# Performance work log

Measured on AMD Instinct MI355X. Metric: run time of the kernel, lower is better.

The kernel has to match this reference:

```python
import jax, jax.numpy as jnp
import numpy as np

DIM = 1024
HEADS = 16
HEAD_DIM = DIM // HEADS


def setup_inputs() -> dict:
    key = jax.random.key(0)
    k_x, k_qkv, k_ow, k_ob = jax.random.split(key, 4)
    x = jax.random.normal(k_x, (2, 2048, DIM), dtype=jnp.float32)
    # nn.Linear(dim, 3*dim, bias=False): weight shape [3*dim, dim], y = x @ W.T
    w_qkv = jax.random.normal(k_qkv, (3 * DIM, DIM), dtype=jnp.float32) * (DIM ** -0.5)
    # nn.Linear(dim, dim) with bias
    w_o = jax.random.normal(k_ow, (DIM, DIM), dtype=jnp.float32) * (DIM ** -0.5)
    b_o = jax.random.normal(k_ob, (DIM,), dtype=jnp.float32) * 0.02
    return {"x": x, "w_qkv": w_qkv, "w_o": w_o, "b_o": b_o}


def reference(x, w_qkv, w_o, b_o):
    b, n, _ = x.shape
    scale = DIM ** -0.5  # NOTE: source scales by full dim, not head dim
    # qkv projection: [b, n, 3*dim]
    qkv = jnp.einsum('bnd,ed->bne', x, w_qkv)
    # 'b n (qkv h d) -> qkv b h n d'
    qkv = qkv.reshape(b, n, 3, HEADS, HEAD_DIM)
    q = jnp.transpose(qkv[:, :, 0], (0, 2, 1, 3))  # [b, h, n, d]
    k = jnp.transpose(qkv[:, :, 1], (0, 2, 1, 3))
    v = jnp.transpose(qkv[:, :, 2], (0, 2, 1, 3))
    scores = jnp.einsum('bhqd,bhkd->bhqk', q, k) * scale  # [b, h, n, n]
    attn = jax.nn.softmax(scores, axis=-1)
    out = jnp.einsum('bhqk,bhkd->bhqd', attn, v)  # [b, h, n, d]
    out = jnp.transpose(out, (0, 2, 1, 3)).reshape(b, n, DIM)  # 'b h n d -> b n (h d)'
    out = jnp.einsum('bnd,ed->bne', out, w_o) + b_o
    return out
```

## Files before the change

kernel.cpp:

```cpp
#include <hip/hip_runtime.h>
#include <stdint.h>


#define DIM 1024
#define SEQ 2048
#define BATCH 2
#define ROWS 4096
#define RSTRIDE 3072

typedef __bf16 bf16_t;
typedef bf16_t bf16x4 __attribute__((ext_vector_type(4)));
typedef bf16_t bf16x8 __attribute__((ext_vector_type(8)));
typedef float f32x4 __attribute__((ext_vector_type(4)));

__device__ __forceinline__ ushort f2bf(float f) {
    uint32_t u;
    __builtin_memcpy(&u, &f, 4);
    uint32_t r = (u + 0x7fffu + ((u >> 16) & 1u)) >> 16;
    return (ushort)r;
}

__device__ __forceinline__ void store_out(ushort* p, float v) { *p = f2bf(v); }
__device__ __forceinline__ void store_out(float* p, float v) { *p = v; }

__device__ __forceinline__ void gl_lds16(const void* g, void* l) {
    __builtin_amdgcn_global_load_lds(
        (const __attribute__((address_space(1))) void*)g,
        (__attribute__((address_space(3))) void*)l, 16, 0, 0);
}

__global__ __launch_bounds__(256) void cvt_kernel(
    const float* __restrict__ src, ushort* __restrict__ dst) {
    int i = (blockIdx.x * 256 + threadIdx.x) * 8;
    float4 a = *(const float4*)(src + i);
    float4 b = *(const float4*)(src + i + 4);
    uint4 u;
    u.x = (uint)f2bf(a.x) | ((uint)f2bf(a.y) << 16);
    u.y = (uint)f2bf(a.z) | ((uint)f2bf(a.w) << 16);
    u.z = (uint)f2bf(b.x) | ((uint)f2bf(b.y) << 16);
    u.w = (uint)f2bf(b.z) | ((uint)f2bf(b.w) << 16);
    *(uint4*)(dst + i) = u;
}

template <typename OutT>
__global__ __launch_bounds__(256) void gemm_bt_kernel(
    const ushort* __restrict__ A, const ushort* __restrict__ B,
    const float* __restrict__ bias, OutT* __restrict__ C,
    int M, int N, int K) {
    __shared__ __align__(16) ushort sA[128 * 32];
    __shared__ __align__(16) ushort sB[128 * 32];

    const int tid = threadIdx.x;
    const int lane = tid & 63, w = tid >> 6;
    const int quad = lane >> 4, l15 = lane & 15;
    const int wm = (w >> 1) * 64, wn = (w & 1) * 64;
    const int bm = blockIdx.y, bn = blockIdx.x;

    f32x4 acc[4][4];
#pragma unroll
    for (int i = 0; i < 4; i++)
#pragma unroll
        for (int j = 0; j < 4; j++) acc[i][j] = (f32x4){0.f, 0.f, 0.f, 0.f};

    const ushort* Abase = A + (size_t)(bm * 128) * K;
    const ushort* Bbase = B + (size_t)(bn * 128) * K;
    const int rr = lane >> 2, c16 = lane & 3;

    for (int kk = 0; kk < K; kk += 32) {
        __syncthreads();
#pragma unroll
        for (int t = 0; t < 2; t++) {
            int row = w * 32 + t * 16;
            gl_lds16(Abase + (size_t)(row + rr) * K + kk + c16 * 8, sA + row * 32);
            gl_lds16(Bbase + (size_t)(row + rr) * K + kk + c16 * 8, sB + row * 32);
        }
        __syncthreads();

        bf16x8 af[4], bfr[4];
#pragma unroll
        for (int i = 0; i < 4; i++)
            af[i] = *(const bf16x8*)((const bf16_t*)sA + (wm + i * 16 + l15) * 32 + quad * 8);
#pragma unroll
        for (int j = 0; j < 4; j++)
            bfr[j] = *(const bf16x8*)((const bf16_t*)sB + (wn + j * 16 + l15) * 32 + quad * 8);
#pragma unroll
        for (int i = 0; i < 4; i++)
#pragma unroll
            for (int j = 0; j < 4; j++)
                acc[i][j] = __builtin_amdgcn_mfma_f32_16x16x32_bf16(
                    af[i], bfr[j], acc[i][j], 0, 0, 0);
    }

#pragma unroll
    for (int i = 0; i < 4; i++)
#pragma unroll
        for (int j = 0; j < 4; j++) {
            int col = bn * 128 + wn + j * 16 + l15;
            float bv = bias ? bias[col] : 0.f;
#pragma unroll
            for (int r = 0; r < 4; r++) {
                int row = bm * 128 + wm + i * 16 + quad * 4 + r;
                store_out(&C[(size_t)row * N + col], acc[i][j][r] + bv);
            }
        }
}

__global__ __launch_bounds__(512) void flash_attn_kernel(
    const ushort* __restrict__ qkv, ushort* __restrict__ out) {
    __shared__ __align__(16) ushort sK[64 * 72];
    __shared__ __align__(16) ushort sVt[64 * 72];
    __shared__ __align__(16) ushort sP[128 * 68];

    const int tid = threadIdx.x;
    const int lane = tid & 63, w = tid >> 6;
    const int quad = lane >> 4, l15 = lane & 15;
    const int bh = blockIdx.y, b = bh >> 4, h = bh & 15;
    const int q0 = blockIdx.x * 128;
    const ushort* qkvb = qkv + (size_t)b * SEQ * RSTRIDE + h * 64;

    const ushort* qrow = qkvb + (size_t)(q0 + w * 16 + l15) * RSTRIDE;
    const bf16x8 aq0 = *(const bf16x8*)(qrow + quad * 8);
    const bf16x8 aq1 = *(const bf16x8*)(qrow + 32 + quad * 8);

    const int krow = tid >> 3, kc8 = tid & 7;
    const int vrp = tid & 31, vc4 = tid >> 5;

    uint4 kreg;
    ushort4 va, vb;
    {
        kreg = *(const uint4*)(qkvb + (size_t)krow * RSTRIDE + DIM + kc8 * 8);
        const ushort* v0 = qkvb + (size_t)(2 * vrp) * RSTRIDE + 2 * DIM + vc4 * 4;
        va = *(const ushort4*)v0;
        vb = *(const ushort4*)(v0 + RSTRIDE);
    }

    f32x4 l_acc = (f32x4){0.f, 0.f, 0.f, 0.f};
    f32x4 o[4];
#pragma unroll
    for (int j = 0; j < 4; j++) o[j] = (f32x4){0.f, 0.f, 0.f, 0.f};

    bf16x8 vones;
#pragma unroll
    for (int e = 0; e < 8; e++) vones[e] = (bf16_t)1.0f;

    const float c_exp = 0.04508422f;

    uint* vt32 = (uint*)sVt;
    for (int kb = 0; kb < SEQ; kb += 64) {
        *(uint4*)(sK + krow * 72 + kc8 * 8) = kreg;
        vt32[(vc4 * 4 + 0) * 36 + vrp] = (uint)va.x | ((uint)vb.x << 16);
        vt32[(vc4 * 4 + 1) * 36 + vrp] = (uint)va.y | ((uint)vb.y << 16);
        vt32[(vc4 * 4 + 2) * 36 + vrp] = (uint)va.z | ((uint)vb.z << 16);
        vt32[(vc4 * 4 + 3) * 36 + vrp] = (uint)va.w | ((uint)vb.w << 16);
        __syncthreads();

        int nkb = (kb + 64 < SEQ) ? kb + 64 : kb;
        {
            kreg = *(const uint4*)(qkvb + (size_t)(nkb + krow) * RSTRIDE + DIM + kc8 * 8);
            const ushort* v0 =
                qkvb + (size_t)(nkb + 2 * vrp) * RSTRIDE + 2 * DIM + vc4 * 4;
            va = *(const ushort4*)v0;
            vb = *(const ushort4*)(v0 + RSTRIDE);
        }

        f32x4 s[4];
#pragma unroll
        for (int j = 0; j < 4; j++) {
            const ushort* kp = sK + (j * 16 + l15) * 72;
            bf16x8 bk0 = *(const bf16x8*)(kp + quad * 8);
            bf16x8 bk1 = *(const bf16x8*)(kp + 32 + quad * 8);
            f32x4 z = (f32x4){0.f, 0.f, 0.f, 0.f};
            z = __builtin_amdgcn_mfma_f32_16x16x32_bf16(aq0, bk0, z, 0, 0, 0);
            z = __builtin_amdgcn_mfma_f32_16x16x32_bf16(aq1, bk1, z, 0, 0, 0);
            s[j] = z;
        }

#pragma unroll
        for (int j = 0; j < 4; j++)
#pragma unroll
            for (int r = 0; r < 4; r++) {
                float p = __builtin_amdgcn_exp2f(s[j][r] * c_exp);
                sP[(w * 16 + quad * 4 + r) * 68 + j * 16 + l15] = f2bf(p);
            }

        const bf16_t* pp = (const bf16_t*)sP + (w * 16 + l15) * 68;
        bf16x4 pl0 = *(const bf16x4*)(pp + quad * 8);
        bf16x4 ph0 = *(const bf16x4*)(pp + quad * 8 + 4);
        bf16x4 pl1 = *(const bf16x4*)(pp + 32 + quad * 8);
        bf16x4 ph1 = *(const bf16x4*)(pp + 32 + quad * 8 + 4);
        bf16x8 pa0 = __builtin_shufflevector(pl0, ph0, 0, 1, 2, 3, 4, 5, 6, 7);
        bf16x8 pa1 = __builtin_shufflevector(pl1, ph1, 0, 1, 2, 3, 4, 5, 6, 7);
        l_acc = __builtin_amdgcn_mfma_f32_16x16x32_bf16(pa0, vones, l_acc, 0, 0, 0);
        l_acc = __builtin_amdgcn_mfma_f32_16x16x32_bf16(pa1, vones, l_acc, 0, 0, 0);
#pragma unroll
        for (int j = 0; j < 4; j++) {
            const bf16_t* vp = (const bf16_t*)sVt + (j * 16 + l15) * 72;
            bf16x8 bv0 = *(const bf16x8*)(vp + quad * 8);
            bf16x8 bv1 = *(const bf16x8*)(vp + 32 + quad * 8);
            o[j] = __builtin_amdgcn_mfma_f32_16x16x32_bf16(pa0, bv0, o[j], 0, 0, 0);
            o[j] = __builtin_amdgcn_mfma_f32_16x16x32_bf16(pa1, bv1, o[j], 0, 0, 0);
        }
        __syncthreads();
    }

#pragma unroll
    for (int r = 0; r < 4; r++) {
        float inv = 1.f / l_acc[r];
        int qrow_i = q0 + w * 16 + quad * 4 + r;
#pragma unroll
        for (int j = 0; j < 4; j++) {
            out[(size_t)(b * SEQ + qrow_i) * DIM + h * 64 + j * 16 + l15] =
                f2bf(o[j][r] * inv);
        }
    }
}

extern "C" void kernel_launch(void* const* d_in, const int* in_sizes, int n_in,
                              void* d_out, int out_size, void* d_ws, size_t ws_size,
                              hipStream_t stream) {
    const float* x = (const float*)d_in[0];
    const float* w_qkv = (const float*)d_in[1];
    const float* w_o = (const float*)d_in[2];
    const float* b_o = (const float*)d_in[3];
    float* out = (float*)d_out;

    ushort* qkv = (ushort*)d_ws;
    ushort* attn = qkv + (size_t)ROWS * 3 * DIM;
    ushort* xb = attn + (size_t)ROWS * DIM;
    ushort* wqkvb = xb + (size_t)ROWS * DIM;
    ushort* wob = wqkvb + (size_t)3 * DIM * DIM;

    dim3 blk(256);
    cvt_kernel<<<ROWS * DIM / 2048, blk, 0, stream>>>(x, xb);
    cvt_kernel<<<3 * DIM * DIM / 2048, blk, 0, stream>>>(w_qkv, wqkvb);
    cvt_kernel<<<DIM * DIM / 2048, blk, 0, stream>>>(w_o, wob);

    gemm_bt_kernel<ushort><<<dim3(3 * DIM / 128, ROWS / 128), blk, 0, stream>>>(
        xb, wqkvb, nullptr, qkv, ROWS, 3 * DIM, DIM);
    flash_attn_kernel<<<dim3(SEQ / 128, BATCH * 16), dim3(512), 0, stream>>>(qkv, attn);
    gemm_bt_kernel<float><<<dim3(DIM / 128, ROWS / 128), blk, 0, stream>>>(
        attn, wob, b_o, out, ROWS, DIM, DIM);
}
```

Measured before the change: 223.7 us.

## Double K-tile depth in GEMM with XOR swizzle and widen attention key block

The GEMM now stages 64-wide K slices instead of 32, using an XOR swizzle on the shared-memory column chunk to avoid bank conflicts, which halves the number of barrier pairs per tile. The attention kernel processes 128 keys per iteration instead of 64, with wider uint4 V loads and a reworked transposed-V layout, again halving the barrier and loop overhead. In exchange, shared memory per block grows, which may lower occupancy, and the extra S tiles raise register pressure.

```diff
diff --git a/kernel.cpp b/kernel.cpp
--- a/kernel.cpp
+++ b/kernel.cpp
@@ -47,8 +47,8 @@
     const ushort* __restrict__ A, const ushort* __restrict__ B,
     const float* __restrict__ bias, OutT* __restrict__ C,
     int M, int N, int K) {
-    __shared__ __align__(16) ushort sA[128 * 32];
-    __shared__ __align__(16) ushort sB[128 * 32];
+    __shared__ __align__(16) ushort sA[128 * 64];
+    __shared__ __align__(16) ushort sB[128 * 64];
 
     const int tid = threadIdx.x;
     const int lane = tid & 63, w = tid >> 6;
@@ -64,31 +64,39 @@
 
     const ushort* Abase = A + (size_t)(bm * 128) * K;
     const ushort* Bbase = B + (size_t)(bn * 128) * K;
-    const int rr = lane >> 2, c16 = lane & 3;
-
-    for (int kk = 0; kk < K; kk += 32) {
-        __syncthreads();
-#pragma unroll
-        for (int t = 0; t < 2; t++) {
-            int row = w * 32 + t * 16;
-            gl_lds16(Abase + (size_t)(row + rr) * K + kk + c16 * 8, sA + row * 32);
-            gl_lds16(Bbase + (size_t)(row + rr) * K + kk + c16 * 8, sB + row * 32);
-        }
-        __syncthreads();
-
-        bf16x8 af[4], bfr[4];
-#pragma unroll
-        for (int i = 0; i < 4; i++)
-            af[i] = *(const bf16x8*)((const bf16_t*)sA + (wm + i * 16 + l15) * 32 + quad * 8);
-#pragma unroll
-        for (int j = 0; j < 4; j++)
-            bfr[j] = *(const bf16x8*)((const bf16_t*)sB + (wn + j * 16 + l15) * 32 + quad * 8);
-#pragma unroll
-        for (int i = 0; i < 4; i++)
+    const int rd = lane >> 3, c8 = lane & 7;
+    const int sw = l15 & 7;
+
+    for (int kk = 0; kk < K; kk += 64) {
+        __syncthreads();
+#pragma unroll
+        for (int t = 0; t < 4; t++) {
+            int row = w * 32 + t * 8;
+            gl_lds16(Abase + (size_t)(row + rd) * K + kk + ((c8 ^ rd) * 8),
+                     sA + row * 64);
+            gl_lds16(Bbase + (size_t)(row + rd) * K + kk + ((c8 ^ rd) * 8),
+                     sB + row * 64);
+        }
+        __syncthreads();
+
+#pragma unroll
+        for (int kh = 0; kh < 2; kh++) {
+            bf16x8 af[4], bfr[4];
+#pragma unroll
+            for (int i = 0; i < 4; i++)
+                af[i] = *(const bf16x8*)((const bf16_t*)sA +
+                        (wm + i * 16 + l15) * 64 + (((kh * 4 + quad) ^ sw) * 8));
 #pragma unroll
             for (int j = 0; j < 4; j++)
-                acc[i][j] = __builtin_amdgcn_mfma_f32_16x16x32_bf16(
-                    af[i], bfr[j], acc[i][j], 0, 0, 0);
+                bfr[j] = *(const bf16x8*)((const bf16_t*)sB +
+                        (wn + j * 16 + l15) * 64 + (((kh * 4 + quad) ^ sw) * 8));
+#pragma unroll
+            for (int i = 0; i < 4; i++)
+#pragma unroll
+                for (int j = 0; j < 4; j++)
+                    acc[i][j] = __builtin_amdgcn_mfma_f32_16x16x32_bf16(
+                        af[i], bfr[j], acc[i][j], 0, 0, 0);
+        }
     }
 
 #pragma unroll
@@ -107,8 +115,8 @@
 
 __global__ __launch_bounds__(512) void flash_attn_kernel(
     const ushort* __restrict__ qkv, ushort* __restrict__ out) {
-    __shared__ __align__(16) ushort sK[64 * 72];
-    __shared__ __align__(16) ushort sVt[64 * 72];
+    __shared__ __align__(16) ushort sK[128 * 72];
+    __shared__ __align__(16) ushort sVt[64 * 136];
     __shared__ __align__(16) ushort sP[128 * 68];
 
     const int tid = threadIdx.x;
@@ -123,15 +131,16 @@
     const bf16x8 aq1 = *(const bf16x8*)(qrow + 32 + quad * 8);
 
     const int krow = tid >> 3, kc8 = tid & 7;
-    const int vrp = tid & 31, vc4 = tid >> 5;
-
-    uint4 kreg;
-    ushort4 va, vb;
+    const int vrp = tid & 63, vc = tid >> 6;
+
+    uint4 kreg0, kreg1, va, vb;
     {
-        kreg = *(const uint4*)(qkvb + (size_t)krow * RSTRIDE + DIM + kc8 * 8);
-        const ushort* v0 = qkvb + (size_t)(2 * vrp) * RSTRIDE + 2 * DIM + vc4 * 4;
-        va = *(const ushort4*)v0;
-        vb = *(const ushort4*)(v0 + RSTRIDE);
+        const ushort* kp0 = qkvb + (size_t)krow * RSTRIDE + DIM + kc8 * 8;
+        kreg0 = *(const uint4*)kp0;
+        kreg1 = *(const uint4*)(kp0 + (size_t)64 * RSTRIDE);
+        const ushort* v0 = qkvb + (size_t)(2 * vrp) * RSTRIDE + 2 * DIM + vc * 8;
+        va = *(const uint4*)v0;
+        vb = *(const uint4*)(v0 + RSTRIDE);
     }
 
     f32x4 l_acc = (f32x4){0.f, 0.f, 0.f, 0.f};
@@ -146,26 +155,36 @@
     const float c_exp = 0.04508422f;
 
     uint* vt32 = (uint*)sVt;
-    for (int kb = 0; kb < SEQ; kb += 64) {
-        *(uint4*)(sK + krow * 72 + kc8 * 8) = kreg;
-        vt32[(vc4 * 4 + 0) * 36 + vrp] = (uint)va.x | ((uint)vb.x << 16);
-        vt32[(vc4 * 4 + 1) * 36 + vrp] = (uint)va.y | ((uint)vb.y << 16);
-        vt32[(vc4 * 4 + 2) * 36 + vrp] = (uint)va.z | ((uint)vb.z << 16);
-        vt32[(vc4 * 4 + 3) * 36 + vrp] = (uint)va.w | ((uint)vb.w << 16);
-        __syncthreads();
-
-        int nkb = (kb + 64 < SEQ) ? kb + 64 : kb;
+    for (int kb = 0; kb < SEQ; kb += 128) {
+        *(uint4*)(sK + krow * 72 + kc8 * 8) = kreg0;
+        *(uint4*)(sK + (krow + 64) * 72 + kc8 * 8) = kreg1;
         {
-            kreg = *(const uint4*)(qkvb + (size_t)(nkb + krow) * RSTRIDE + DIM + kc8 * 8);
+            int base = (vc * 8) * 68 + vrp;
+            vt32[base + 0 * 68] = (va.x & 0xffffu) | (vb.x << 16);
+            vt32[base + 1 * 68] = (va.x >> 16) | (vb.x & 0xffff0000u);
+            vt32[base + 2 * 68] = (va.y & 0xffffu) | (vb.y << 16);
+            vt32[base + 3 * 68] = (va.y >> 16) | (vb.y & 0xffff0000u);
+            vt32[base + 4 * 68] = (va.z & 0xffffu) | (vb.z << 16);
+            vt32[base + 5 * 68] = (va.z >> 16) | (vb.z & 0xffff0000u);
+            vt32[base + 6 * 68] = (va.w & 0xffffu) | (vb.w << 16);
+            vt32[base + 7 * 68] = (va.w >> 16) | (vb.w & 0xffff0000u);
+        }
+        __syncthreads();
+
+        int nkb = (kb + 128 < SEQ) ? kb + 128 : kb;
+        {
+            const ushort* kp0 = qkvb + (size_t)(nkb + krow) * RSTRIDE + DIM + kc8 * 8;
+            kreg0 = *(const uint4*)kp0;
+            kreg1 = *(const uint4*)(kp0 + (size_t)64 * RSTRIDE);
             const ushort* v0 =
-                qkvb + (size_t)(nkb + 2 * vrp) * RSTRIDE + 2 * DIM + vc4 * 4;
-            va = *(const ushort4*)v0;
-            vb = *(const ushort4*)(v0 + RSTRIDE);
-        }
-
-        f32x4 s[4];
-#pragma unroll
-        for (int j = 0; j < 4; j++) {
+                qkvb + (size_t)(nkb + 2 * vrp) * RSTRIDE + 2 * DIM + vc * 8;
+            va = *(const uint4*)v0;
+            vb = *(const uint4*)(v0 + RSTRIDE);
+        }
+
+        f32x4 s[8];
+#pragma unroll
+        for (int j = 0; j < 8; j++) {
             const ushort* kp = sK + (j * 16 + l15) * 72;
             bf16x8 bk0 = *(const bf16x8*)(kp + quad * 8);
             bf16x8 bk1 = *(const bf16x8*)(kp + 32 + quad * 8);
@@ -176,29 +195,32 @@
         }
 
 #pragma unroll
-        for (int j = 0; j < 4; j++)
-#pragma unroll
-            for (int r = 0; r < 4; r++) {
-                float p = __builtin_amdgcn_exp2f(s[j][r] * c_exp);
-                sP[(w * 16 + quad * 4 + r) * 68 + j * 16 + l15] = f2bf(p);
+        for (int h2 = 0; h2 < 2; h2++) {
+#pragma unroll
+            for (int j = 0; j < 4; j++)
+#pragma unroll
+                for (int r = 0; r < 4; r++) {
+                    float p = __builtin_amdgcn_exp2f(s[h2 * 4 + j][r] * c_exp);
+                    sP[(w * 16 + quad * 4 + r) * 68 + j * 16 + l15] = f2bf(p);
+                }
+            const bf16_t* pp = (const bf16_t*)sP + (w * 16 + l15) * 68;
+            bf16x4 pl0 = *(const bf16x4*)(pp + quad * 8);
+            bf16x4 ph0 = *(const bf16x4*)(pp + quad * 8 + 4);
+            bf16x4 pl1 = *(const bf16x4*)(pp + 32 + quad * 8);
+            bf16x4 ph1 = *(const bf16x4*)(pp + 32 + quad * 8 + 4);
+            bf16x8 pa0 = __builtin_shufflevector(pl0, ph0, 0, 1, 2, 3, 4, 5, 6, 7);
+            bf16x8 pa1 = __builtin_shufflevector(pl1, ph1, 0, 1, 2, 3, 4, 5, 6, 7);
+            l_acc = __builtin_amdgcn_mfma_f32_16x16x32_bf16(pa0, vones, l_acc, 0, 0, 0);
+            l_acc = __builtin_amdgcn_mfma_f32_16x16x32_bf16(pa1, vones, l_acc, 0, 0, 0);
+#pragma unroll
+            for (int jd = 0; jd < 4; jd++) {
+                const bf16_t* vp =
+                    (const bf16_t*)sVt + (jd * 16 + l15) * 136 + h2 * 64;
+                bf16x8 bv0 = *(const bf16x8*)(vp + quad * 8);
+                bf16x8 bv1 = *(const bf16x8*)(vp + 32 + quad * 8);
+                o[jd] = __builtin_amdgcn_mfma_f32_16x16x32_bf16(pa0, bv0, o[jd], 0, 0, 0);
+                o[jd] = __builtin_amdgcn_mfma_f32_16x16x32_bf16(pa1, bv1, o[jd], 0, 0, 0);
             }
-
-        const bf16_t* pp = (const bf16_t*)sP + (w * 16 + l15) * 68;
-        bf16x4 pl0 = *(const bf16x4*)(pp + quad * 8);
-        bf16x4 ph0 = *(const bf16x4*)(pp + quad * 8 + 4);
-        bf16x4 pl1 = *(const bf16x4*)(pp + 32 + quad * 8);
-        bf16x4 ph1 = *(const bf16x4*)(pp + 32 + quad * 8 + 4);
-        bf16x8 pa0 = __builtin_shufflevector(pl0, ph0, 0, 1, 2, 3, 4, 5, 6, 7);
-        bf16x8 pa1 = __builtin_shufflevector(pl1, ph1, 0, 1, 2, 3, 4, 5, 6, 7);
-        l_acc = __builtin_amdgcn_mfma_f32_16x16x32_bf16(pa0, vones, l_acc, 0, 0, 0);
-        l_acc = __builtin_amdgcn_mfma_f32_16x16x32_bf16(pa1, vones, l_acc, 0, 0, 0);
-#pragma unroll
-        for (int j = 0; j < 4; j++) {
-            const bf16_t* vp = (const bf16_t*)sVt + (j * 16 + l15) * 72;
-            bf16x8 bv0 = *(const bf16x8*)(vp + quad * 8);
-            bf16x8 bv1 = *(const bf16x8*)(vp + 32 + quad * 8);
-            o[j] = __builtin_amdgcn_mfma_f32_16x16x32_bf16(pa0, bv0, o[j], 0, 0, 0);
-            o[j] = __builtin_amdgcn_mfma_f32_16x16x32_bf16(pa1, bv1, o[j], 0, 0, 0);
         }
         __syncthreads();
     }
```

After: 219.1 us. -2.1%, faster.
